# Performance work log

Hardware: AMD Instinct MI355X
Metric: run time of the kernel (lower is better)

The kernel has to match this reference:

```python
import jax, jax.numpy as jnp
import numpy as np
import math

EMBED = 512
KDIM = 512
VDIM = 512
H = 8
HD = EMBED // H
N = 2048
L = 2048
B = 4


def setup_inputs() -> dict:
    key = jax.random.key(0)
    ks = jax.random.split(key, 14)
    s = 1.0 / math.sqrt(EMBED)
    return {
        "q": jax.random.normal(ks[0], (N, B, EMBED), jnp.float32),
        "k": jax.random.normal(ks[1], (L, B, KDIM), jnp.float32),
        "v": jax.random.normal(ks[2], (L, B, VDIM), jnp.float32),
        "pe1": jax.random.normal(ks[3], (B, N, 3), jnp.float32),
        "pe2": jax.random.normal(ks[4], (L, 3), jnp.float32),
        "Wq": jax.random.normal(ks[5], (EMBED, EMBED), jnp.float32) * s,
        "bq": jnp.zeros((EMBED,), jnp.float32),
        "Wk": jax.random.normal(ks[6], (EMBED, KDIM), jnp.float32) * s,
        "bk": jnp.zeros((EMBED,), jnp.float32),
        "Wv": jax.random.normal(ks[7], (EMBED, VDIM), jnp.float32) * s,
        "bv": jnp.zeros((EMBED,), jnp.float32),
        "Wo": jax.random.normal(ks[8], (EMBED, EMBED), jnp.float32) * s,
        "bo": jnp.zeros((EMBED,), jnp.float32),
    }


def reference(q, k, v, pe1, pe2, Wq, bq, Wk, bk, Wv, bv, Wo, bo):
    n, b, _ = q.shape
    l = k.shape[0]
    # projections (nn.Linear: x @ W.T + b)
    qp = q @ Wq.T + bq  # (n, b, E)
    kp = k @ Wk.T + bk  # (l, b, E)
    vp = v @ Wv.T + bv  # (l, b, E)
    # split heads -> (b, H, n, hd)
    qh = qp.reshape(n, b, H, HD).transpose(1, 2, 0, 3)
    kh = kp.reshape(l, b, H, HD).transpose(1, 2, 0, 3)
    vh = vp.reshape(l, b, H, HD).transpose(1, 2, 0, 3)
    # relative PE bias: (b, n, l), broadcast over heads
    pe_scores = jnp.einsum('bnc,lc->bnl', pe1, pe2)[:, None, :, :]
    scores = (jnp.einsum('bhnd,bhld->bhnl', qh, kh) + pe_scores) / math.sqrt(HD)
    attn = jax.nn.softmax(scores, axis=-1)
    out = jnp.einsum('bhnl,bhld->bhnd', attn, vh)  # (b, H, n, hd)
    out = out.transpose(2, 0, 1, 3).reshape(n, b, EMBED)
    return out @ Wo.T + bo
```

## Files before the change

kernel.cpp:

```cpp
#include <hip/hip_runtime.h>
#include <math.h>

#define EMBED 512
#define HDIM 64
#define NHEADS 8
#define SEQ_N 2048
#define SEQ_L 2048
#define BATCH 4
#define MROWS (SEQ_N*BATCH)
#define BE (BATCH*EMBED)

#define QSCALE 0.18033688f

typedef _Float16 f16;
typedef _Float16 half8 __attribute__((ext_vector_type(8)));
typedef _Float16 half4 __attribute__((ext_vector_type(4)));
typedef _Float16 half2v __attribute__((ext_vector_type(2)));
typedef float floatx4 __attribute__((ext_vector_type(4)));
typedef float floatx16 __attribute__((ext_vector_type(16)));

static __device__ inline float fast_exp2(float x) {
#if __has_builtin(__builtin_amdgcn_exp2f)
  return __builtin_amdgcn_exp2f(x);
#else
  return __expf(x * 0.69314718056f);
#endif
}

static __device__ inline half2v pk2(float a, float b) {
#if __has_builtin(__builtin_amdgcn_cvt_pkrtz)
  return __builtin_bit_cast(half2v, __builtin_amdgcn_cvt_pkrtz(a, b));
#else
  half2v o; o[0] = (f16)a; o[1] = (f16)b; return o;
#endif
}

static __device__ inline void gload16(const void* g, void* l) {
  __builtin_amdgcn_global_load_lds(
      (__attribute__((address_space(1))) void*)(g),
      (__attribute__((address_space(3))) void*)(l), 16, 0, 0);
}

__global__ __launch_bounds__(256) void cvt_all(const float* __restrict__ q,
                                               const float* __restrict__ k,
                                               const float* __restrict__ v,
                                               const float* __restrict__ Wq,
                                               const float* __restrict__ Wk,
                                               const float* __restrict__ Wv,
                                               const float* __restrict__ Wo,
                                               f16* __restrict__ qb, f16* __restrict__ kb,
                                               f16* __restrict__ vb, f16* __restrict__ Wb) {
  const long TOK = (long)MROWS * EMBED;
  const long WSZ = (long)EMBED * EMBED;
  int y = blockIdx.y;
  long i = ((long)blockIdx.x * 256 + threadIdx.x) * 4;
  if (y < 3) {
    if (i < TOK) {
      const float* s = y == 0 ? q : y == 1 ? k : v;
      f16* d = y == 0 ? qb : y == 1 ? kb : vb;
      float4 f = *reinterpret_cast<const float4*>(s + i);
      half4 o; o[0] = (f16)f.x; o[1] = (f16)f.y; o[2] = (f16)f.z; o[3] = (f16)f.w;
      *reinterpret_cast<half4*>(d + i) = o;
    }
  } else {
    if (i < 4 * WSZ) {
      int sel = (int)(i >> 18);
      long off = i & (WSZ - 1);
      const float* s = sel == 0 ? Wq : sel == 1 ? Wk : sel == 2 ? Wv : Wo;
      float4 f = *reinterpret_cast<const float4*>(s + off);
      half4 o; o[0] = (f16)f.x; o[1] = (f16)f.y; o[2] = (f16)f.z; o[3] = (f16)f.w;
      *reinterpret_cast<half4*>(Wb + i) = o;
    }
  }
}

__global__ __launch_bounds__(256) void gemm_qkv(const f16* __restrict__ A0,
                                                const f16* __restrict__ A1,
                                                const f16* __restrict__ A2,
                                                const f16* __restrict__ W0,
                                                const f16* __restrict__ W1,
                                                const f16* __restrict__ W2,
                                                const float* __restrict__ b0,
                                                const float* __restrict__ b1,
                                                const float* __restrict__ b2,
                                                f16* __restrict__ C0, f16* __restrict__ C1,
                                                f16* __restrict__ C2t) {
  __shared__ alignas(16) f16 As[2][128 * 32];
  __shared__ alignas(16) f16 Bs[2][128 * 32];
  const int sel = blockIdx.y >> 2;
  const f16* A = sel == 0 ? A0 : sel == 1 ? A1 : A2;
  const f16* Bt = sel == 0 ? W0 : sel == 1 ? W1 : W2;
  const float* bias = sel == 0 ? b0 : sel == 1 ? b1 : b2;
  const float scl = sel == 0 ? QSCALE : 1.0f;
  const int tid = threadIdx.x;
  const int wave = tid >> 6, lane = tid & 63, quad = lane >> 4, l16 = lane & 15;
  const int wm = wave & 1, wn = wave >> 1;
  const long m0 = (long)blockIdx.x * 128;
  const long n0 = (long)(blockIdx.y & 3) * 128;
  const int srow = lane >> 2;
  const int scol = (lane & 3) * 8;

  const f16* Ag0 = A + (m0 + wave * 32 + srow) * EMBED + scol;
  const f16* Ag1 = A + (m0 + wave * 32 + 16 + srow) * EMBED + scol;
  const f16* Bg0 = Bt + (n0 + wave * 32 + srow) * EMBED + scol;
  const f16* Bg1 = Bt + (n0 + wave * 32 + 16 + srow) * EMBED + scol;

  gload16(Ag0, &As[0][(wave * 32) * 32]);
  gload16(Ag1, &As[0][(wave * 32 + 16) * 32]);
  gload16(Bg0, &Bs[0][(wave * 32) * 32]);
  gload16(Bg1, &Bs[0][(wave * 32 + 16) * 32]);
  floatx4 acc[4][4] = {};
  asm volatile("s_waitcnt vmcnt(0)" ::: "memory");
  __builtin_amdgcn_s_barrier();

#pragma unroll
  for (int ks = 0; ks < 16; ++ks) {
    const int cur = ks & 1;
    if (ks + 1 < 16) {
      const int k1 = (ks + 1) * 32;
      gload16(Ag0 + k1, &As[cur ^ 1][(wave * 32) * 32]);
      gload16(Ag1 + k1, &As[cur ^ 1][(wave * 32 + 16) * 32]);
      gload16(Bg0 + k1, &Bs[cur ^ 1][(wave * 32) * 32]);
      gload16(Bg1 + k1, &Bs[cur ^ 1][(wave * 32 + 16) * 32]);
    }
    half8 af[4], bf[4];
#pragma unroll
    for (int i = 0; i < 4; ++i)
      af[i] = *reinterpret_cast<const half8*>(&As[cur][(wm * 64 + i * 16 + l16) * 32 + quad * 8]);
#pragma unroll
    for (int j = 0; j < 4; ++j)
      bf[j] = *reinterpret_cast<const half8*>(&Bs[cur][(wn * 64 + j * 16 + l16) * 32 + quad * 8]);
#pragma unroll
    for (int i = 0; i < 4; ++i)
#pragma unroll
      for (int j = 0; j < 4; ++j)
        acc[i][j] = __builtin_amdgcn_mfma_f32_16x16x32_f16(af[i], bf[j], acc[i][j], 0, 0, 0);
    if (ks + 1 < 16) {
      asm volatile("s_waitcnt vmcnt(0)" ::: "memory");
      __builtin_amdgcn_s_barrier();
    }
  }
#pragma unroll
  for (int i = 0; i < 4; ++i)
#pragma unroll
    for (int r = 0; r < 4; ++r) {
      long row = m0 + wm * 64 + i * 16 + quad * 4 + r;
#pragma unroll
      for (int j = 0; j < 4; ++j) {
        long col = n0 + wn * 64 + j * 16 + l16;
        float val = (acc[i][j][r] + bias[col]) * scl;
        if (sel == 2) {
          long bq = row & 3, ltok = row >> 2;
          long hh = col >> 6, dd = col & 63;
          C2t[(((bq << 3) + hh) * 64 + dd) * 2048 + ltok] = (f16)val;
        } else {
          f16* C = sel == 0 ? C0 : C1;
          C[row * EMBED + col] = (f16)val;
        }
      }
    }
}

__global__ __launch_bounds__(256) void gemm_out(const f16* __restrict__ A,
                                                const f16* __restrict__ Bt,
                                                const float* __restrict__ bias,
                                                float* __restrict__ C) {
  __shared__ alignas(16) f16 As[2][128 * 32];
  __shared__ alignas(16) f16 Bs[2][64 * 32];
  const int tid = threadIdx.x;
  const int wave = tid >> 6, lane = tid & 63, quad = lane >> 4, l16 = lane & 15;
  const long m0 = (long)blockIdx.x * 128;
  const long n0 = (long)blockIdx.y * 64;
  const int srow = lane >> 2;
  const int scol = (lane & 3) * 8;

  const f16* Ag0 = A + (m0 + wave * 32 + srow) * EMBED + scol;
  const f16* Ag1 = A + (m0 + wave * 32 + 16 + srow) * EMBED + scol;
  const f16* Bg0 = Bt + (n0 + wave * 16 + srow) * EMBED + scol;

  gload16(Ag0, &As[0][(wave * 32) * 32]);
  gload16(Ag1, &As[0][(wave * 32 + 16) * 32]);
  gload16(Bg0, &Bs[0][(wave * 16) * 32]);
  floatx4 acc[2][4] = {};
  asm volatile("s_waitcnt vmcnt(0)" ::: "memory");
  __builtin_amdgcn_s_barrier();

#pragma unroll
  for (int ks = 0; ks < 16; ++ks) {
    const int cur = ks & 1;
    if (ks + 1 < 16) {
      const int k1 = (ks + 1) * 32;
      gload16(Ag0 + k1, &As[cur ^ 1][(wave * 32) * 32]);
      gload16(Ag1 + k1, &As[cur ^ 1][(wave * 32 + 16) * 32]);
      gload16(Bg0 + k1, &Bs[cur ^ 1][(wave * 16) * 32]);
    }
    half8 af[2], bf[4];
#pragma unroll
    for (int i = 0; i < 2; ++i)
      af[i] = *reinterpret_cast<const half8*>(&As[cur][(wave * 32 + i * 16 + l16) * 32 + quad * 8]);
#pragma unroll
    for (int j = 0; j < 4; ++j)
      bf[j] = *reinterpret_cast<const half8*>(&Bs[cur][(j * 16 + l16) * 32 + quad * 8]);
#pragma unroll
    for (int i = 0; i < 2; ++i)
#pragma unroll
      for (int j = 0; j < 4; ++j)
        acc[i][j] = __builtin_amdgcn_mfma_f32_16x16x32_f16(af[i], bf[j], acc[i][j], 0, 0, 0);
    if (ks + 1 < 16) {
      asm volatile("s_waitcnt vmcnt(0)" ::: "memory");
      __builtin_amdgcn_s_barrier();
    }
  }
#pragma unroll
  for (int i = 0; i < 2; ++i)
#pragma unroll
    for (int r = 0; r < 4; ++r) {
      long row = m0 + wave * 32 + i * 16 + quad * 4 + r;
#pragma unroll
      for (int j = 0; j < 4; ++j) {
        long col = n0 + j * 16 + l16;
        C[row * EMBED + col] = acc[i][j][r] + bias[col];
      }
    }
}

#define KST 88
#define VST 136
#define NCHUNK (SEQ_L / 128)
#define LDSB (128 * KST * 2 + 64 * VST * 2)
__global__ __launch_bounds__(512, 4) void attn_flash(const f16* __restrict__ qp,
                                                     const f16* __restrict__ kp,
                                                     const f16* __restrict__ vt,
                                                     const float* __restrict__ pe1,
                                                     const float* __restrict__ pe2,
                                                     f16* __restrict__ ao) {
  __shared__ alignas(16) unsigned char smem[LDSB];
  f16* Ks = reinterpret_cast<f16*>(smem);
  f16* Vt = reinterpret_cast<f16*>(smem + 128 * KST * 2);
  float* comb = reinterpret_cast<float*>(smem);
  const int tid = threadIdx.x, wave = tid >> 6, lane = tid & 63;
  const int m = lane & 31, h = lane >> 5;
  const int strip = wave & 3, half = wave >> 2;
  const int n0 = blockIdx.x * 128;
  const int b = blockIdx.y >> 3, hd = blockIdx.y & 7;
  const long headoff = (long)b * EMBED + hd * HDIM;
  const long vhead = (long)blockIdx.y * 64 * 2048;

  for (int c = tid; c < 1024; c += 512) {
    int r = c >> 3, col = (c & 7) * 8;
    *reinterpret_cast<uint4*>(&Ks[r * KST + col]) =
        *reinterpret_cast<const uint4*>(qp + (long)(n0 + r) * BE + headoff + col);
    int rv = c >> 4, cv = (c & 15) * 8;
    *reinterpret_cast<uint4*>(&Vt[rv * VST + cv]) =
        *reinterpret_cast<const uint4*>(vt + vhead + (long)rv * 2048 + 0 + cv);
  }
  {
    const uint4 z4 = {0, 0, 0, 0};
    const uint2 z2 = {0, 0};
    int r = tid >> 2, s = tid & 3;
    if (s == 0) *reinterpret_cast<uint2*>(&Ks[r * KST + 68]) = z2;
    else if (s == 1) *reinterpret_cast<uint4*>(&Ks[r * KST + 72]) = z4;
    else if (s == 2) *reinterpret_cast<uint4*>(&Ks[r * KST + 80]) = z4;
  }
  if (tid < 128) {
    long base = ((long)b * SEQ_N + n0 + tid) * 3;
    half4 v8;
    v8[0] = (f16)(pe1[base + 0] * QSCALE);
    v8[1] = (f16)(pe1[base + 1] * QSCALE);
    v8[2] = (f16)(pe1[base + 2] * QSCALE);
    v8[3] = (f16)0.f;
    *reinterpret_cast<half4*>(&Ks[tid * KST + 64]) = v8;
  }
  __syncthreads();

  half8 qf[5];
#pragma unroll
  for (int e = 0; e < 5; ++e)
    qf[e] = *reinterpret_cast<const half8*>(&Ks[(strip * 32 + m) * KST + e * 16 + h * 8]);
  __syncthreads();

  for (int c = tid; c < 1024; c += 512) {
    int r = c >> 3, col = (c & 7) * 8;
    *reinterpret_cast<uint4*>(&Ks[r * KST + col]) =
        *reinterpret_cast<const uint4*>(kp + (long)(0 + r) * BE + headoff + col);
  }
  if (tid < 128) {
    long bb = (long)(0 + tid) * 3;
    half4 p2;
    p2[0] = (f16)pe2[bb + 0]; p2[1] = (f16)pe2[bb + 1];
    p2[2] = (f16)pe2[bb + 2]; p2[3] = (f16)0.f;
    *reinterpret_cast<half4*>(&Ks[tid * KST + 64]) = p2;
  }

  floatx16 oacc[2] = {};
  float lpart = 0.f;

#pragma unroll 1
  for (int c = 0; c < NCHUNK; ++c) {
    __syncthreads();

    uint4 kreg0, kreg1, vreg0, vreg1;
    float p2x, p2y, p2z;
    const bool pf = (c + 1 < NCHUNK);
    if (pf) {
      const int l0 = (c + 1) * 128;
      {
        int r = tid >> 3, col = (tid & 7) * 8;
        kreg0 = *reinterpret_cast<const uint4*>(kp + (long)(l0 + r) * BE + headoff + col);
        int rv = tid >> 4, cv = (tid & 15) * 8;
        vreg0 = *reinterpret_cast<const uint4*>(vt + vhead + (long)rv * 2048 + l0 + cv);
      }
      {
        int c2 = tid + 512;
        int r = c2 >> 3, col = (c2 & 7) * 8;
        kreg1 = *reinterpret_cast<const uint4*>(kp + (long)(l0 + r) * BE + headoff + col);
        int rv = c2 >> 4, cv = (c2 & 15) * 8;
        vreg1 = *reinterpret_cast<const uint4*>(vt + vhead + (long)rv * 2048 + l0 + cv);
      }
      if (tid < 128) {
        long bb = (long)(l0 + tid) * 3;
        p2x = pe2[bb + 0]; p2y = pe2[bb + 1]; p2z = pe2[bb + 2];
      }
      __builtin_amdgcn_sched_barrier(0);
    }

#pragma unroll
    for (int tt = 0; tt < 2; ++tt) {
      const int t = half * 2 + tt;
      floatx16 st = {};
#pragma unroll
      for (int e = 0; e < 5; ++e) {
        half8 kf = *reinterpret_cast<const half8*>(&Ks[(t * 32 + m) * KST + e * 16 + h * 8]);
        st = __builtin_amdgcn_mfma_f32_32x32x16_f16(kf, qf[e], st, 0, 0, 0);
      }
      float p[16];
#pragma unroll
      for (int r = 0; r < 16; ++r) {
        p[r] = fast_exp2(st[r]);
        lpart += p[r];
      }
#pragma unroll
      for (int s = 0; s < 4; ++s) {
        half2v u0 = pk2(p[4 * s + 0], p[4 * s + 1]);
        half2v u1 = pk2(p[4 * s + 2], p[4 * s + 3]);
        half4 bp;
        bp[0] = u0[0]; bp[1] = u0[1]; bp[2] = u1[0]; bp[3] = u1[1];
        int lcol = t * 32 + s * 8 + h * 4;
#pragma unroll
        for (int dt = 0; dt < 2; ++dt) {
          half4 vf = *reinterpret_cast<const half4*>(&Vt[(dt * 32 + m) * VST + lcol]);
          oacc[dt] = __builtin_amdgcn_mfma_f32_32x32x8f16(vf, bp, oacc[dt], 0, 0, 0);
        }
      }
    }
    __syncthreads();

    if (pf) {
      {
        int r = tid >> 3, col = (tid & 7) * 8;
        *reinterpret_cast<uint4*>(&Ks[r * KST + col]) = kreg0;
        int rv = tid >> 4, cv = (tid & 15) * 8;
        *reinterpret_cast<uint4*>(&Vt[rv * VST + cv]) = vreg0;
      }
      {
        int c2 = tid + 512;
        int r = c2 >> 3, col = (c2 & 7) * 8;
        *reinterpret_cast<uint4*>(&Ks[r * KST + col]) = kreg1;
        int rv = c2 >> 4, cv = (c2 & 15) * 8;
        *reinterpret_cast<uint4*>(&Vt[rv * VST + cv]) = vreg1;
      }
      if (tid < 128) {
        half4 p2;
        p2[0] = (f16)p2x; p2[1] = (f16)p2y; p2[2] = (f16)p2z; p2[3] = (f16)0.f;
        *reinterpret_cast<half4*>(&Ks[tid * KST + 64]) = p2;
      }
    }
  }

  lpart += __shfl_xor(lpart, 32);

  if (half == 1) {
    float* dst = comb + (strip * 64 + lane) * 33;
#pragma unroll
    for (int dt = 0; dt < 2; ++dt)
#pragma unroll
      for (int x = 0; x < 16; ++x) dst[dt * 16 + x] = oacc[dt][x];
    dst[32] = lpart;
  }
  __syncthreads();
  if (half == 0) {
    const float* src = comb + (strip * 64 + lane) * 33;
#pragma unroll
    for (int dt = 0; dt < 2; ++dt)
#pragma unroll
      for (int x = 0; x < 16; ++x) oacc[dt][x] += src[dt * 16 + x];
    float inv = 1.f / (lpart + src[32]);
    long qrow = n0 + strip * 32 + m;
#pragma unroll
    for (int dt = 0; dt < 2; ++dt)
#pragma unroll
      for (int g = 0; g < 4; ++g) {
        half4 o4;
#pragma unroll
        for (int x = 0; x < 4; ++x) o4[x] = (f16)(oacc[dt][4 * g + x] * inv);
        int d = dt * 32 + 8 * g + 4 * h;
        *reinterpret_cast<half4*>(ao + qrow * BE + headoff + d) = o4;
      }
  }
}

extern "C" void kernel_launch(void* const* d_in, const int* in_sizes, int n_in,
                              void* d_out, int out_size, void* d_ws, size_t ws_size,
                              hipStream_t stream) {
  const float* q   = (const float*)d_in[0];
  const float* k   = (const float*)d_in[1];
  const float* v   = (const float*)d_in[2];
  const float* pe1 = (const float*)d_in[3];
  const float* pe2 = (const float*)d_in[4];
  const float* Wq  = (const float*)d_in[5];
  const float* bq  = (const float*)d_in[6];
  const float* Wk  = (const float*)d_in[7];
  const float* bk  = (const float*)d_in[8];
  const float* Wv  = (const float*)d_in[9];
  const float* bv  = (const float*)d_in[10];
  const float* Wo  = (const float*)d_in[11];
  const float* bo  = (const float*)d_in[12];
  float* out = (float*)d_out;

  f16* ws = (f16*)d_ws;
  const long TOK = (long)MROWS * EMBED;
  const long WSZ = (long)EMBED * EMBED;
  f16* qb  = ws;
  f16* kb  = qb + TOK;
  f16* vb  = kb + TOK;
  f16* Wqb = vb + TOK;
  f16* Wkb = Wqb + WSZ;
  f16* Wvb = Wkb + WSZ;
  f16* Wob = Wvb + WSZ;
  f16* qpb = Wob + WSZ;
  f16* kpb = qpb + TOK;
  f16* vtb = kpb + TOK;
  f16* aob = vtb + TOK;

  cvt_all<<<dim3(4096, 4), 256, 0, stream>>>(q, k, v, Wq, Wk, Wv, Wo, qb, kb, vb, Wqb);

  gemm_qkv<<<dim3(MROWS / 128, 12), 256, 0, stream>>>(qb, kb, vb, Wqb, Wkb, Wvb,
                                                      bq, bk, bv, qpb, kpb, vtb);

  attn_flash<<<dim3(SEQ_N / 128, BATCH * NHEADS), 512, 0, stream>>>(qpb, kpb, vtb, pe1, pe2, aob);

  gemm_out<<<dim3(MROWS / 128, EMBED / 64), 256, 0, stream>>>(aob, Wob, bo, out);
}
```

Baseline: 215.5 us.

## Split key sequence across two wave groups per block in attention kernel

The attention kernel now launches 1024 threads per block as two 512-thread groups. Each group processes half of the key/value sequence in its own LDS region, and the partial outputs and row sums are combined through shared memory at the end. The register-staged prefetch of the next K/V chunk is removed in favour of direct global-to-LDS copies after each chunk. This aims to increase parallelism per block and shorten the serial chunk loop. In exchange it loses the load/compute overlap, uses twice the LDS per block, adds an extra reduction step, and sets launch bounds that may limit registers per thread.

```diff
diff --git a/kernel.cpp b/kernel.cpp
--- a/kernel.cpp
+++ b/kernel.cpp
@@ -226,50 +226,55 @@
 
 #define KST 88
 #define VST 136
-#define NCHUNK (SEQ_L / 128)
-#define LDSB (128 * KST * 2 + 64 * VST * 2)
-__global__ __launch_bounds__(512, 4) void attn_flash(const f16* __restrict__ qp,
-                                                     const f16* __restrict__ kp,
-                                                     const f16* __restrict__ vt,
-                                                     const float* __restrict__ pe1,
-                                                     const float* __restrict__ pe2,
-                                                     f16* __restrict__ ao) {
+#define GBYTES (128 * KST * 2 + 64 * VST * 2)
+#define LDSB (2 * GBYTES)
+#define NCHUNK2 (SEQ_L / 128 / 2)
+__global__ __launch_bounds__(1024, 8) void attn_flash(const f16* __restrict__ qp,
+                                                      const f16* __restrict__ kp,
+                                                      const f16* __restrict__ vt,
+                                                      const float* __restrict__ pe1,
+                                                      const float* __restrict__ pe2,
+                                                      f16* __restrict__ ao) {
   __shared__ alignas(16) unsigned char smem[LDSB];
-  f16* Ks = reinterpret_cast<f16*>(smem);
-  f16* Vt = reinterpret_cast<f16*>(smem + 128 * KST * 2);
+  const int tid = threadIdx.x, wave = tid >> 6, lane = tid & 63;
+  const int grp = tid >> 9;
+  const int gtid = tid & 511;
+  const int wv = wave & 7;
+  const int m = lane & 31, h = lane >> 5;
+  const int strip = wv & 3, half = wv >> 2;
+  f16* Ks = reinterpret_cast<f16*>(smem + grp * GBYTES);
+  f16* Vt = reinterpret_cast<f16*>(smem + grp * GBYTES + 128 * KST * 2);
   float* comb = reinterpret_cast<float*>(smem);
-  const int tid = threadIdx.x, wave = tid >> 6, lane = tid & 63;
-  const int m = lane & 31, h = lane >> 5;
-  const int strip = wave & 3, half = wave >> 2;
   const int n0 = blockIdx.x * 128;
   const int b = blockIdx.y >> 3, hd = blockIdx.y & 7;
   const long headoff = (long)b * EMBED + hd * HDIM;
   const long vhead = (long)blockIdx.y * 64 * 2048;
-
-  for (int c = tid; c < 1024; c += 512) {
+  const int lbase = grp * 1024;
+
+  for (int c = gtid; c < 1024; c += 512) {
     int r = c >> 3, col = (c & 7) * 8;
     *reinterpret_cast<uint4*>(&Ks[r * KST + col]) =
         *reinterpret_cast<const uint4*>(qp + (long)(n0 + r) * BE + headoff + col);
     int rv = c >> 4, cv = (c & 15) * 8;
     *reinterpret_cast<uint4*>(&Vt[rv * VST + cv]) =
-        *reinterpret_cast<const uint4*>(vt + vhead + (long)rv * 2048 + 0 + cv);
+        *reinterpret_cast<const uint4*>(vt + vhead + (long)rv * 2048 + lbase + cv);
   }
   {
     const uint4 z4 = {0, 0, 0, 0};
     const uint2 z2 = {0, 0};
-    int r = tid >> 2, s = tid & 3;
+    int r = gtid >> 2, s = gtid & 3;
     if (s == 0) *reinterpret_cast<uint2*>(&Ks[r * KST + 68]) = z2;
     else if (s == 1) *reinterpret_cast<uint4*>(&Ks[r * KST + 72]) = z4;
     else if (s == 2) *reinterpret_cast<uint4*>(&Ks[r * KST + 80]) = z4;
   }
-  if (tid < 128) {
-    long base = ((long)b * SEQ_N + n0 + tid) * 3;
+  if (gtid < 128) {
+    long base = ((long)b * SEQ_N + n0 + gtid) * 3;
     half4 v8;
     v8[0] = (f16)(pe1[base + 0] * QSCALE);
     v8[1] = (f16)(pe1[base + 1] * QSCALE);
     v8[2] = (f16)(pe1[base + 2] * QSCALE);
     v8[3] = (f16)0.f;
-    *reinterpret_cast<half4*>(&Ks[tid * KST + 64]) = v8;
+    *reinterpret_cast<half4*>(&Ks[gtid * KST + 64]) = v8;
   }
   __syncthreads();
 
@@ -279,51 +284,25 @@
     qf[e] = *reinterpret_cast<const half8*>(&Ks[(strip * 32 + m) * KST + e * 16 + h * 8]);
   __syncthreads();
 
-  for (int c = tid; c < 1024; c += 512) {
+  for (int c = gtid; c < 1024; c += 512) {
     int r = c >> 3, col = (c & 7) * 8;
     *reinterpret_cast<uint4*>(&Ks[r * KST + col]) =
-        *reinterpret_cast<const uint4*>(kp + (long)(0 + r) * BE + headoff + col);
-  }
-  if (tid < 128) {
-    long bb = (long)(0 + tid) * 3;
+        *reinterpret_cast<const uint4*>(kp + (long)(lbase + r) * BE + headoff + col);
+  }
+  if (gtid < 128) {
+    long bb = (long)(lbase + gtid) * 3;
     half4 p2;
     p2[0] = (f16)pe2[bb + 0]; p2[1] = (f16)pe2[bb + 1];
     p2[2] = (f16)pe2[bb + 2]; p2[3] = (f16)0.f;
-    *reinterpret_cast<half4*>(&Ks[tid * KST + 64]) = p2;
+    *reinterpret_cast<half4*>(&Ks[gtid * KST + 64]) = p2;
   }
 
   floatx16 oacc[2] = {};
   float lpart = 0.f;
 
 #pragma unroll 1
-  for (int c = 0; c < NCHUNK; ++c) {
+  for (int c = 0; c < NCHUNK2; ++c) {
     __syncthreads();
-
-    uint4 kreg0, kreg1, vreg0, vreg1;
-    float p2x, p2y, p2z;
-    const bool pf = (c + 1 < NCHUNK);
-    if (pf) {
-      const int l0 = (c + 1) * 128;
-      {
-        int r = tid >> 3, col = (tid & 7) * 8;
-        kreg0 = *reinterpret_cast<const uint4*>(kp + (long)(l0 + r) * BE + headoff + col);
-        int rv = tid >> 4, cv = (tid & 15) * 8;
-        vreg0 = *reinterpret_cast<const uint4*>(vt + vhead + (long)rv * 2048 + l0 + cv);
-      }
-      {
-        int c2 = tid + 512;
-        int r = c2 >> 3, col = (c2 & 7) * 8;
-        kreg1 = *reinterpret_cast<const uint4*>(kp + (long)(l0 + r) * BE + headoff + col);
-        int rv = c2 >> 4, cv = (c2 & 15) * 8;
-        vreg1 = *reinterpret_cast<const uint4*>(vt + vhead + (long)rv * 2048 + l0 + cv);
-      }
-      if (tid < 128) {
-        long bb = (long)(l0 + tid) * 3;
-        p2x = pe2[bb + 0]; p2y = pe2[bb + 1]; p2z = pe2[bb + 2];
-      }
-      __builtin_amdgcn_sched_barrier(0);
-    }
-
 #pragma unroll
     for (int tt = 0; tt < 2; ++tt) {
       const int t = half * 2 + tt;
@@ -354,25 +333,22 @@
       }
     }
     __syncthreads();
-
-    if (pf) {
-      {
-        int r = tid >> 3, col = (tid & 7) * 8;
-        *reinterpret_cast<uint4*>(&Ks[r * KST + col]) = kreg0;
-        int rv = tid >> 4, cv = (tid & 15) * 8;
-        *reinterpret_cast<uint4*>(&Vt[rv * VST + cv]) = vreg0;
-      }
-      {
-        int c2 = tid + 512;
-        int r = c2 >> 3, col = (c2 & 7) * 8;
-        *reinterpret_cast<uint4*>(&Ks[r * KST + col]) = kreg1;
-        int rv = c2 >> 4, cv = (c2 & 15) * 8;
-        *reinterpret_cast<uint4*>(&Vt[rv * VST + cv]) = vreg1;
-      }
-      if (tid < 128) {
+    if (c + 1 < NCHUNK2) {
+      const int l0 = lbase + (c + 1) * 128;
+      for (int cc = gtid; cc < 1024; cc += 512) {
+        int r = cc >> 3, col = (cc & 7) * 8;
+        *reinterpret_cast<uint4*>(&Ks[r * KST + col]) =
+            *reinterpret_cast<const uint4*>(kp + (long)(l0 + r) * BE + headoff + col);
+        int rv = cc >> 4, cv = (cc & 15) * 8;
+        *reinterpret_cast<uint4*>(&Vt[rv * VST + cv]) =
+            *reinterpret_cast<const uint4*>(vt + vhead + (long)rv * 2048 + l0 + cv);
+      }
+      if (gtid < 128) {
+        long bb = (long)(l0 + gtid) * 3;
         half4 p2;
-        p2[0] = (f16)p2x; p2[1] = (f16)p2y; p2[2] = (f16)p2z; p2[3] = (f16)0.f;
-        *reinterpret_cast<half4*>(&Ks[tid * KST + 64]) = p2;
+        p2[0] = (f16)pe2[bb + 0]; p2[1] = (f16)pe2[bb + 1];
+        p2[2] = (f16)pe2[bb + 2]; p2[3] = (f16)0.f;
+        *reinterpret_cast<half4*>(&Ks[gtid * KST + 64]) = p2;
       }
     }
   }
@@ -380,7 +356,7 @@
   lpart += __shfl_xor(lpart, 32);
 
   if (half == 1) {
-    float* dst = comb + (strip * 64 + lane) * 33;
+    float* dst = comb + (((grp << 2) + strip) * 64 + lane) * 33;
 #pragma unroll
     for (int dt = 0; dt < 2; ++dt)
 #pragma unroll
@@ -389,7 +365,24 @@
   }
   __syncthreads();
   if (half == 0) {
-    const float* src = comb + (strip * 64 + lane) * 33;
+    float* slot = comb + (((grp << 2) + strip) * 64 + lane) * 33;
+    if (grp == 0) {
+#pragma unroll
+      for (int dt = 0; dt < 2; ++dt)
+#pragma unroll
+        for (int x = 0; x < 16; ++x) oacc[dt][x] += slot[dt * 16 + x];
+      lpart += slot[32];
+    } else {
+#pragma unroll
+      for (int dt = 0; dt < 2; ++dt)
+#pragma unroll
+        for (int x = 0; x < 16; ++x) slot[dt * 16 + x] += oacc[dt][x];
+      slot[32] += lpart;
+    }
+  }
+  __syncthreads();
+  if (half == 0 && grp == 0) {
+    const float* src = comb + ((4 + strip) * 64 + lane) * 33;
 #pragma unroll
     for (int dt = 0; dt < 2; ++dt)
 #pragma unroll
@@ -447,7 +440,7 @@
   gemm_qkv<<<dim3(MROWS / 128, 12), 256, 0, stream>>>(qb, kb, vb, Wqb, Wkb, Wvb,
                                                       bq, bk, bv, qpb, kpb, vtb);
 
-  attn_flash<<<dim3(SEQ_N / 128, BATCH * NHEADS), 512, 0, stream>>>(qpb, kpb, vtb, pe1, pe2, aob);
+  attn_flash<<<dim3(SEQ_N / 128, BATCH * NHEADS), 1024, 0, stream>>>(qpb, kpb, vtb, pe1, pe2, aob);
 
   gemm_out<<<dim3(MROWS / 128, EMBED / 64), 256, 0, stream>>>(aob, Wob, bo, out);
 }
```

Result: slower. 468.7 us (+117.5%).

## Move V transpose into separate LDS-tiled kernel and drop register prefetch in attention

Applied to the files above, without the earlier changes.

The V projection now writes row-major output, and a new vtrans kernel transposes it per (batch, head) through XOR-swizzled shared memory so the global writes coalesce, replacing the scattered 2-byte transposed stores in the QKV GEMM epilogue. The attention kernel's register-staged prefetch of the next K/V/pe2 chunk is replaced by direct global-to-LDS copies after the compute barrier. The aim is to remove the uncoalesced store cost and lower register pressure, at the price of an extra launch, an extra read and write of V, and load latency no longer hidden behind the MFMA work.

```diff
diff --git a/kernel.cpp b/kernel.cpp
--- a/kernel.cpp
+++ b/kernel.cpp
@@ -84,7 +84,7 @@
                                                 const float* __restrict__ b1,
                                                 const float* __restrict__ b2,
                                                 f16* __restrict__ C0, f16* __restrict__ C1,
-                                                f16* __restrict__ C2t) {
+                                                f16* __restrict__ C2) {
   __shared__ alignas(16) f16 As[2][128 * 32];
   __shared__ alignas(16) f16 Bs[2][128 * 32];
   const int sel = blockIdx.y >> 2;
@@ -92,6 +92,7 @@
   const f16* Bt = sel == 0 ? W0 : sel == 1 ? W1 : W2;
   const float* bias = sel == 0 ? b0 : sel == 1 ? b1 : b2;
   const float scl = sel == 0 ? QSCALE : 1.0f;
+  f16* C = sel == 0 ? C0 : sel == 1 ? C1 : C2;
   const int tid = threadIdx.x;
   const int wave = tid >> 6, lane = tid & 63, quad = lane >> 4, l16 = lane & 15;
   const int wm = wave & 1, wn = wave >> 1;
@@ -149,16 +150,36 @@
       for (int j = 0; j < 4; ++j) {
         long col = n0 + wn * 64 + j * 16 + l16;
         float val = (acc[i][j][r] + bias[col]) * scl;
-        if (sel == 2) {
-          long bq = row & 3, ltok = row >> 2;
-          long hh = col >> 6, dd = col & 63;
-          C2t[(((bq << 3) + hh) * 64 + dd) * 2048 + ltok] = (f16)val;
-        } else {
-          f16* C = sel == 0 ? C0 : C1;
-          C[row * EMBED + col] = (f16)val;
-        }
-      }
-    }
+        C[row * EMBED + col] = (f16)val;
+      }
+    }
+}
+
+__global__ __launch_bounds__(256) void vtrans(const f16* __restrict__ vp,
+                                              f16* __restrict__ vt) {
+  __shared__ alignas(16) f16 T[128 * 64];
+  const int tid = threadIdx.x;
+  const int l0 = blockIdx.x * 128;
+  const int bh = blockIdx.y;
+  const int b = bh >> 3, h = bh & 7;
+  for (int c = tid; c < 1024; c += 256) {
+    int r = c >> 3, seg = c & 7;
+    uint4 v = *reinterpret_cast<const uint4*>(
+        vp + ((long)(l0 + r) * 4 + b) * EMBED + h * 64 + seg * 8);
+    int dseg = seg ^ ((r >> 3) & 7);
+    *reinterpret_cast<uint4*>(&T[r * 64 + dseg * 8]) = v;
+  }
+  __syncthreads();
+  for (int c = tid; c < 1024; c += 256) {
+    int d = c >> 4, seg = c & 15;
+    half8 o;
+#pragma unroll
+    for (int i = 0; i < 8; ++i) {
+      int r = seg * 8 + i;
+      o[i] = T[r * 64 + (d ^ (((r >> 3) & 7) << 3))];
+    }
+    *reinterpret_cast<half8*>(vt + ((long)bh * 64 + d) * 2048 + l0 + seg * 8) = o;
+  }
 }
 
 __global__ __launch_bounds__(256) void gemm_out(const f16* __restrict__ A,
@@ -298,32 +319,6 @@
 #pragma unroll 1
   for (int c = 0; c < NCHUNK; ++c) {
     __syncthreads();
-
-    uint4 kreg0, kreg1, vreg0, vreg1;
-    float p2x, p2y, p2z;
-    const bool pf = (c + 1 < NCHUNK);
-    if (pf) {
-      const int l0 = (c + 1) * 128;
-      {
-        int r = tid >> 3, col = (tid & 7) * 8;
-        kreg0 = *reinterpret_cast<const uint4*>(kp + (long)(l0 + r) * BE + headoff + col);
-        int rv = tid >> 4, cv = (tid & 15) * 8;
-        vreg0 = *reinterpret_cast<const uint4*>(vt + vhead + (long)rv * 2048 + l0 + cv);
-      }
-      {
-        int c2 = tid + 512;
-        int r = c2 >> 3, col = (c2 & 7) * 8;
-        kreg1 = *reinterpret_cast<const uint4*>(kp + (long)(l0 + r) * BE + headoff + col);
-        int rv = c2 >> 4, cv = (c2 & 15) * 8;
-        vreg1 = *reinterpret_cast<const uint4*>(vt + vhead + (long)rv * 2048 + l0 + cv);
-      }
-      if (tid < 128) {
-        long bb = (long)(l0 + tid) * 3;
-        p2x = pe2[bb + 0]; p2y = pe2[bb + 1]; p2z = pe2[bb + 2];
-      }
-      __builtin_amdgcn_sched_barrier(0);
-    }
-
 #pragma unroll
     for (int tt = 0; tt < 2; ++tt) {
       const int t = half * 2 + tt;
@@ -354,24 +349,21 @@
       }
     }
     __syncthreads();
-
-    if (pf) {
-      {
-        int r = tid >> 3, col = (tid & 7) * 8;
-        *reinterpret_cast<uint4*>(&Ks[r * KST + col]) = kreg0;
-        int rv = tid >> 4, cv = (tid & 15) * 8;
-        *reinterpret_cast<uint4*>(&Vt[rv * VST + cv]) = vreg0;
-      }
-      {
-        int c2 = tid + 512;
-        int r = c2 >> 3, col = (c2 & 7) * 8;
-        *reinterpret_cast<uint4*>(&Ks[r * KST + col]) = kreg1;
-        int rv = c2 >> 4, cv = (c2 & 15) * 8;
-        *reinterpret_cast<uint4*>(&Vt[rv * VST + cv]) = vreg1;
+    if (c + 1 < NCHUNK) {
+      const int l0 = (c + 1) * 128;
+      for (int cc = tid; cc < 1024; cc += 512) {
+        int r = cc >> 3, col = (cc & 7) * 8;
+        *reinterpret_cast<uint4*>(&Ks[r * KST + col]) =
+            *reinterpret_cast<const uint4*>(kp + (long)(l0 + r) * BE + headoff + col);
+        int rv = cc >> 4, cv = (cc & 15) * 8;
+        *reinterpret_cast<uint4*>(&Vt[rv * VST + cv]) =
+            *reinterpret_cast<const uint4*>(vt + vhead + (long)rv * 2048 + l0 + cv);
       }
       if (tid < 128) {
+        long bb = (long)(l0 + tid) * 3;
         half4 p2;
-        p2[0] = (f16)p2x; p2[1] = (f16)p2y; p2[2] = (f16)p2z; p2[3] = (f16)0.f;
+        p2[0] = (f16)pe2[bb + 0]; p2[1] = (f16)pe2[bb + 1];
+        p2[2] = (f16)pe2[bb + 2]; p2[3] = (f16)0.f;
         *reinterpret_cast<half4*>(&Ks[tid * KST + 64]) = p2;
       }
     }
@@ -441,11 +433,14 @@
   f16* kpb = qpb + TOK;
   f16* vtb = kpb + TOK;
   f16* aob = vtb + TOK;
+  f16* vpb = aob;
 
   cvt_all<<<dim3(4096, 4), 256, 0, stream>>>(q, k, v, Wq, Wk, Wv, Wo, qb, kb, vb, Wqb);
 
   gemm_qkv<<<dim3(MROWS / 128, 12), 256, 0, stream>>>(qb, kb, vb, Wqb, Wkb, Wvb,
-                                                      bq, bk, bv, qpb, kpb, vtb);
+                                                      bq, bk, bv, qpb, kpb, vpb);
+
+  vtrans<<<dim3(SEQ_L / 128, BATCH * NHEADS), 256, 0, stream>>>(vpb, vtb);
 
   attn_flash<<<dim3(SEQ_N / 128, BATCH * NHEADS), 512, 0, stream>>>(qpb, kpb, vtb, pe1, pe2, aob);
 
```

Measured after the change: 210.5 us. -2.3%, faster.
